# Kernel optimization log

Hardware: AMD Instinct MI355X
Metric: run time of the kernel (lower is better)

## Reference

```python
import jax, jax.numpy as jnp
import numpy as np

BNK, L, DIN, DOUT, NREL = 1280, 64, 512, 256, 40

def setup_inputs() -> dict:
    key = jax.random.key(0)
    ks = jax.random.split(key, 10)
    rep = jax.random.normal(ks[0], (BNK, L, DIN), dtype=jnp.float32)
    # adj_arc_in[..., 0] = flattened sentence index, adj_arc_in[..., 1] = head token position
    sent = jnp.broadcast_to(jnp.arange(BNK, dtype=jnp.int64)[:, None], (BNK, L))
    head = jax.random.randint(ks[1], (BNK, L), 0, L, dtype=jnp.int64)
    adj_arc_in = jnp.stack([sent, head], axis=-1)  # [BNK, L, 2]
    adj_lab_in = jax.random.randint(ks[2], (BNK, L), 0, NREL, dtype=jnp.int64)
    adj_mask_in = (jax.random.uniform(ks[3], (BNK, L)) < 0.9).astype(jnp.float32)
    adj_mask_loop = jnp.ones((BNK, L), dtype=jnp.float32)
    mask = jnp.ones((BNK, L), dtype=jnp.float32)
    # parameters (xavier-ish init)
    W_in = jax.random.normal(ks[4], (DIN, DOUT), dtype=jnp.float32) * (2.0 / (DIN + DOUT)) ** 0.5
    b_in = jnp.zeros((NREL, DOUT), dtype=jnp.float32)
    W_gate_in = jax.random.uniform(ks[5], (DIN, 1), dtype=jnp.float32)
    b_gate_in = jnp.ones((NREL, 1), dtype=jnp.float32)
    W_self = jax.random.normal(ks[6], (DIN, DOUT), dtype=jnp.float32) * (2.0 / (DIN + DOUT)) ** 0.5
    W_gate_self = jax.random.uniform(ks[7], (DIN, 1), dtype=jnp.float32)
    return {"rep": rep, "adj_mask_in": adj_mask_in, "adj_mask_loop": adj_mask_loop,
            "mask": mask, "W_in": W_in, "b_in": b_in, "W_gate_in": W_gate_in,
            "b_gate_in": b_gate_in, "W_self": W_self, "W_gate_self": W_gate_self,
            "adj_arc_in": adj_arc_in, "adj_lab_in": adj_lab_in}

def reference(rep, adj_mask_in, adj_mask_loop, mask, W_in, b_in, W_gate_in,
              b_gate_in, W_self, W_gate_self, adj_arc_in, adj_lab_in):
    bnk, l, din = rep.shape
    dout = W_in.shape[1]
    rep_ = rep.reshape(bnk * l, din)                    # [M, Din]
    idx = adj_arc_in[..., 0].reshape(-1) * l + adj_arc_in[..., 1].reshape(-1)  # [M]
    lab = adj_lab_in.reshape(-1)                        # [M]
    # in-arc potential: gather projected head token, add relation-typed bias
    in_pot = (rep_ @ W_in)[idx] + b_in[lab]             # [M, Dout]
    in_gate = (rep_ @ W_gate_in)[idx, 0] + b_gate_in[lab, 0]  # [M]
    # self-loop potential
    self_pot = rep_ @ W_self                            # [M, Dout]
    self_gate = (rep_ @ W_gate_self)[:, 0]              # [M]
    pots = jnp.stack([in_pot, self_pot], axis=1)        # [M, 2, Dout]
    gates = jnp.stack([in_gate, self_gate], axis=1)     # [M, 2]
    msoft = jnp.stack([adj_mask_in.reshape(-1), adj_mask_loop.reshape(-1)], axis=1)  # [M, 2]
    # original multiplies by mask_soft twice: potentials * mask_soft * (sigmoid(gate) * mask_soft)
    w = jax.nn.sigmoid(gates) * msoft * msoft           # [M, 2]
    res = jax.nn.relu(jnp.einsum('mdk,md->mk', pots, w))  # [M, Dout]
    res = res.reshape(bnk, l, dout) * mask.reshape(bnk, l)[..., None]
    return res
```

## Files before the change

kernel.cpp:

```cpp
#include <hip/hip_runtime.h>


#define BNK   1280
#define LTOK  64
#define DIN   512
#define DOUT  256
#define NCAT  512
#define TPB   512
#define BK    32
#define NCHUNK (DIN / BK)
#define A_STRIDE 56

typedef __attribute__((ext_vector_type(4))) float f32x4;
typedef __attribute__((ext_vector_type(8))) short s16x8;

__device__ __forceinline__ unsigned short f2bf(float f) {
  unsigned u = __float_as_uint(f);
  unsigned r = (u + 0x7FFFu + ((u >> 16) & 1u)) >> 16;
  return (unsigned short)r;
}
__device__ __forceinline__ float bf2f(unsigned short h) {
  return __uint_as_float(((unsigned)h) << 16);
}
__device__ __forceinline__ float sigmoidf_(float x) {
  return 1.0f / (1.0f + __expf(-x));
}

__global__ __launch_bounds__(256) void wprep_kernel(const float* __restrict__ W_in,
                                                    const float* __restrict__ W_self,
                                                    unsigned short* __restrict__ Wt) {
  __shared__ float tile[32][33];
  const int t  = threadIdx.x;
  const int c0 = (blockIdx.x & 15) * 32;
  const int k0 = (blockIdx.x >> 4) * 32;
  const float* src = (c0 < DOUT) ? W_in : W_self;
  const int cadj   = (c0 < DOUT) ? c0 : (c0 - DOUT);
  {
    const int kk = t >> 3;
    const int cc = (t & 7) * 4;
    const float4 v = *(const float4*)(src + (size_t)(k0 + kk) * DOUT + cadj + cc);
    tile[kk][cc + 0] = v.x; tile[kk][cc + 1] = v.y;
    tile[kk][cc + 2] = v.z; tile[kk][cc + 3] = v.w;
  }
  __syncthreads();
  {
    const int cc = t >> 3;
    const int kk = (t & 7) * 4;
    ushort4 o;
    o.x = f2bf(tile[kk + 0][cc]); o.y = f2bf(tile[kk + 1][cc]);
    o.z = f2bf(tile[kk + 2][cc]); o.w = f2bf(tile[kk + 3][cc]);
    *(ushort4*)(Wt + (size_t)(c0 + cc) * DIN + k0 + kk) = o;
  }
}

__global__ __launch_bounds__(TPB) void gcn_kernel(
    const float* __restrict__ rep,
    const float* __restrict__ adj_mask_in,
    const float* __restrict__ adj_mask_loop,
    const float* __restrict__ maskp,
    const float* __restrict__ b_in,
    const float* __restrict__ w_gate_in,
    const float* __restrict__ b_gate_in,
    const float* __restrict__ w_gate_self,
    const int* __restrict__ arc,
    const int* __restrict__ lab,
    const unsigned short* __restrict__ Wt,
    float* __restrict__ out)
{
  __shared__ __align__(16) char smem[41728];
  unsigned short* As  = (unsigned short*)(smem);
  unsigned short* Ws  = (unsigned short*)(smem + 7168);
  unsigned short* Pin = (unsigned short*)(smem);
  unsigned short* Psf = (unsigned short*)(smem + 16384);
  float* wgi  = (float*)(smem);
  float* wgs  = (float*)(smem + 2048);
  float* part = (float*)(smem + 4096);
  float* gld  = (float*)(smem + 39936);
  float* winl = (float*)(smem + 40448);
  float* wsfl = (float*)(smem + 40704);
  float* mskl = (float*)(smem + 40960);
  int*   hdl  = (int*)(smem + 41216);
  int*   lbl  = (int*)(smem + 41472);

  const int b    = blockIdx.x;
  const int t    = threadIdx.x;
  const int wave = t >> 6;
  const int lane = t & 63;
  const int nlo  = lane & 15;
  const int quad = lane >> 4;

  wgi[t] = w_gate_in[t];
  wgs[t] = w_gate_self[t];
  __syncthreads();
  {
    const int r = t >> 3, p = t & 7;
    const float* row = rep + (size_t)(b * LTOK + r) * DIN;
    float si = 0.f, ss = 0.f;
    #pragma unroll 8
    for (int j = 0; j < 64; ++j) {
      const int k = p + j * 8;
      const float a = row[k];
      si += a * wgi[k];
      ss += a * wgs[k];
    }
    part[t * 2 + 0] = si;
    part[t * 2 + 1] = ss;
  }
  __syncthreads();
  if (t < 128) {
    const int r = t >> 1, g = t & 1;
    float s = 0.f;
    #pragma unroll
    for (int p = 0; p < 8; ++p) s += part[(r * 8 + p) * 2 + g];
    gld[r * 2 + g] = s;
  }

  f32x4 acc[4][4];
  #pragma unroll
  for (int i = 0; i < 4; ++i)
    #pragma unroll
    for (int j = 0; j < 4; ++j) {
      f32x4 z = {0.f, 0.f, 0.f, 0.f};
      acc[i][j] = z;
    }

  for (int kc = 0; kc < NCHUNK; ++kc) {
    __syncthreads();
    const int k0 = kc * BK;

    #pragma unroll
    for (int i = 0; i < 4; ++i) {
      const int u = i * TPB + t;
      const int c = u >> 2;
      const int p = u & 3;
      const int q = p ^ ((c >> 1) & 3);
      const unsigned short* g = Wt + (size_t)c * DIN + k0 + q * 8;
      __builtin_amdgcn_global_load_lds(
          (const __attribute__((address_space(1))) void*)g,
          (__attribute__((address_space(3))) void*)(smem + 7168 + u * 16),
          16, 0, 0);
    }

    {
      const int r  = t >> 3;
      const int kk = (t & 7) * 4;
      const float4 v = *(const float4*)(rep + (size_t)(b * LTOK + r) * DIN + k0 + kk);
      ushort4 o;
      o.x = f2bf(v.x); o.y = f2bf(v.y); o.z = f2bf(v.z); o.w = f2bf(v.w);
      *(ushort4*)(As + r * A_STRIDE + kk) = o;
    }
    __syncthreads();

    s16x8 af[4];
    #pragma unroll
    for (int mt = 0; mt < 4; ++mt)
      af[mt] = *(const s16x8*)(As + (mt * 16 + nlo) * A_STRIDE + quad * 8);

    #pragma unroll
    for (int nt = 0; nt < 4; ++nt) {
      const int c = wave * 64 + nt * 16 + nlo;
      const int p = quad ^ ((c >> 1) & 3);
      const s16x8 bfr = *(const s16x8*)(Ws + c * BK + p * 8);
      #pragma unroll
      for (int mt = 0; mt < 4; ++mt)
        acc[mt][nt] = __builtin_amdgcn_mfma_f32_16x16x32_bf16(af[mt], bfr, acc[mt][nt], 0, 0, 0);
    }
  }

  __syncthreads();

  if (t < LTOK) {
    const int m  = b * LTOK + t;
    const int hd = arc[2 * m + 1];
    const int lb = lab[m];
    const float am = adj_mask_in[m];
    const float al = adj_mask_loop[m];
    winl[t] = sigmoidf_(gld[hd * 2 + 0] + b_gate_in[lb]) * am * am;
    wsfl[t] = sigmoidf_(gld[t * 2 + 1]) * al * al;
    mskl[t] = maskp[m];
    hdl[t]  = hd;
    lbl[t]  = lb;
  }

  for (int s = 0; s < 2; ++s) {
    if (s) __syncthreads();
    const int half = wave >> 2;
    const int wcol = wave & 3;
    if ((wcol >> 1) == s) {
      unsigned short* dst = half ? Psf : Pin;
      const int cb = (wcol & 1) * 64;
      #pragma unroll
      for (int mt = 0; mt < 4; ++mt)
        #pragma unroll
        for (int nt = 0; nt < 4; ++nt)
          #pragma unroll
          for (int r = 0; r < 4; ++r) {
            const int row = mt * 16 + quad * 4 + r;
            const int col = cb + nt * 16 + nlo;
            dst[row * 128 + col] = f2bf(acc[mt][nt][r]);
          }
    }
    __syncthreads();
    #pragma unroll
    for (int i = 0; i < 4; ++i) {
      const int q   = i * TPB + t;
      const int row = q >> 5;
      const int cl  = (q & 31) * 4;
      const int cg  = s * 128 + cl;
      const int hd  = hdl[row];
      const int lb  = lbl[row];
      const float wi = winl[row], ws = wsfl[row], mk = mskl[row];
      const float4 bi = *(const float4*)(b_in + lb * DOUT + cg);
      const ushort4 pi = *(const ushort4*)(Pin + hd * 128 + cl);
      const ushort4 ps = *(const ushort4*)(Psf + row * 128 + cl);
      float4 v;
      v.x = (bf2f(pi.x) + bi.x) * wi + bf2f(ps.x) * ws;
      v.y = (bf2f(pi.y) + bi.y) * wi + bf2f(ps.y) * ws;
      v.z = (bf2f(pi.z) + bi.z) * wi + bf2f(ps.z) * ws;
      v.w = (bf2f(pi.w) + bi.w) * wi + bf2f(ps.w) * ws;
      v.x = fmaxf(v.x, 0.f) * mk; v.y = fmaxf(v.y, 0.f) * mk;
      v.z = fmaxf(v.z, 0.f) * mk; v.w = fmaxf(v.w, 0.f) * mk;
      *(float4*)(out + (size_t)(b * LTOK + row) * DOUT + cg) = v;
    }
  }
}

extern "C" void kernel_launch(void* const* d_in, const int* in_sizes, int n_in,
                              void* d_out, int out_size, void* d_ws, size_t ws_size,
                              hipStream_t stream) {
  const float* rep           = (const float*)d_in[0];
  const float* adj_mask_in   = (const float*)d_in[1];
  const float* adj_mask_loop = (const float*)d_in[2];
  const float* mask          = (const float*)d_in[3];
  const float* W_in          = (const float*)d_in[4];
  const float* b_in          = (const float*)d_in[5];
  const float* W_gate_in     = (const float*)d_in[6];
  const float* b_gate_in     = (const float*)d_in[7];
  const float* W_self        = (const float*)d_in[8];
  const float* W_gate_self   = (const float*)d_in[9];
  const int*   arc           = (const int*)d_in[10];
  const int*   lab           = (const int*)d_in[11];
  float* out = (float*)d_out;
  unsigned short* Wt = (unsigned short*)d_ws;

  wprep_kernel<<<256, 256, 0, stream>>>(W_in, W_self, Wt);
  gcn_kernel<<<BNK, TPB, 0, stream>>>(rep, adj_mask_in, adj_mask_loop, mask, b_in,
                                      W_gate_in, b_gate_in, W_gate_self, arc, lab, Wt, out);
}
```

Measured before the change: 378.7 us.

## Stage full A tile once in LDS and stream W fragments directly from global

The gate-dot pass now also converts each rep row to bf16 and stores the whole 64x512 A tile in swizzled LDS in the same read, so the per-chunk rep reload and conversion inside the K loop go away. B fragments are read straight from global/L2 into registers instead of being staged through LDS with per-chunk barriers, so the K loop has no syncthreads and is fully unrolled. The epilogue writes both projections into LDS with a padded stride in a single pass rather than two halves. The kernel uses more shared memory (about 77KB) and relies on L2 bandwidth for the repeated W reads, with a launch-bounds occupancy hint added.

Result: faster. 357.6 us (-5.6%).

```diff
diff --git a/kernel.cpp b/kernel.cpp
--- a/kernel.cpp
+++ b/kernel.cpp
@@ -5,11 +5,10 @@
 #define LTOK  64
 #define DIN   512
 #define DOUT  256
-#define NCAT  512
 #define TPB   512
-#define BK    32
-#define NCHUNK (DIN / BK)
-#define A_STRIDE 56
+#define PSTR  264
+
+#define SMEM_BYTES 77568
 
 typedef __attribute__((ext_vector_type(4))) float f32x4;
 typedef __attribute__((ext_vector_type(8))) short s16x8;
@@ -53,7 +52,7 @@
   }
 }
 
-__global__ __launch_bounds__(TPB) void gcn_kernel(
+__global__ __launch_bounds__(TPB, 4) void gcn_kernel(
     const float* __restrict__ rep,
     const float* __restrict__ adj_mask_in,
     const float* __restrict__ adj_mask_loop,
@@ -67,20 +66,19 @@
     const unsigned short* __restrict__ Wt,
     float* __restrict__ out)
 {
-  __shared__ __align__(16) char smem[41728];
+  __shared__ __align__(16) char smem[SMEM_BYTES];
   unsigned short* As  = (unsigned short*)(smem);
-  unsigned short* Ws  = (unsigned short*)(smem + 7168);
   unsigned short* Pin = (unsigned short*)(smem);
-  unsigned short* Psf = (unsigned short*)(smem + 16384);
-  float* wgi  = (float*)(smem);
-  float* wgs  = (float*)(smem + 2048);
-  float* part = (float*)(smem + 4096);
-  float* gld  = (float*)(smem + 39936);
-  float* winl = (float*)(smem + 40448);
-  float* wsfl = (float*)(smem + 40704);
-  float* mskl = (float*)(smem + 40960);
-  int*   hdl  = (int*)(smem + 41216);
-  int*   lbl  = (int*)(smem + 41472);
+  unsigned short* Psf = (unsigned short*)(smem + 33792);
+  float* wgi  = (float*)(smem + 67584);
+  float* wgs  = (float*)(smem + 69632);
+  float* part = (float*)(smem + 71680);
+  float* gld  = (float*)(smem + 75776);
+  float* winl = (float*)(smem + 76288);
+  float* wsfl = (float*)(smem + 76544);
+  float* mskl = (float*)(smem + 76800);
+  int*   hdl  = (int*)(smem + 77056);
+  int*   lbl  = (int*)(smem + 77312);
 
   const int b    = blockIdx.x;
   const int t    = threadIdx.x;
@@ -92,21 +90,38 @@
   wgi[t] = w_gate_in[t];
   wgs[t] = w_gate_self[t];
   __syncthreads();
+
   {
     const int r = t >> 3, p = t & 7;
-    const float* row = rep + (size_t)(b * LTOK + r) * DIN;
+    const float* arow = rep + (size_t)(b * LTOK + r) * DIN;
     float si = 0.f, ss = 0.f;
-    #pragma unroll 8
-    for (int j = 0; j < 64; ++j) {
-      const int k = p + j * 8;
-      const float a = row[k];
-      si += a * wgi[k];
-      ss += a * wgs[k];
+    #pragma unroll 4
+    for (int i = 0; i < 8; ++i) {
+      const int kg = p + 8 * i;
+      const int kb = kg * 8;
+      const float4 v0 = *(const float4*)(arow + kb);
+      const float4 v1 = *(const float4*)(arow + kb + 4);
+      const float4 g0 = *(const float4*)(wgi + kb);
+      const float4 g1 = *(const float4*)(wgi + kb + 4);
+      const float4 h0 = *(const float4*)(wgs + kb);
+      const float4 h1 = *(const float4*)(wgs + kb + 4);
+      si += v0.x*g0.x + v0.y*g0.y + v0.z*g0.z + v0.w*g0.w
+          + v1.x*g1.x + v1.y*g1.y + v1.z*g1.z + v1.w*g1.w;
+      ss += v0.x*h0.x + v0.y*h0.y + v0.z*h0.z + v0.w*h0.w
+          + v1.x*h1.x + v1.y*h1.y + v1.z*h1.z + v1.w*h1.w;
+      s16x8 o;
+      o[0] = (short)f2bf(v0.x); o[1] = (short)f2bf(v0.y);
+      o[2] = (short)f2bf(v0.z); o[3] = (short)f2bf(v0.w);
+      o[4] = (short)f2bf(v1.x); o[5] = (short)f2bf(v1.y);
+      o[6] = (short)f2bf(v1.z); o[7] = (short)f2bf(v1.w);
+      const int u = (kg >> 2) * 256 + (kg & 3) * 64 + (r ^ p);
+      *(s16x8*)(As + u * 8) = o;
     }
     part[t * 2 + 0] = si;
     part[t * 2 + 1] = ss;
   }
   __syncthreads();
+
   if (t < 128) {
     const int r = t >> 1, g = t & 1;
     float s = 0.f;
@@ -124,47 +139,26 @@
       acc[i][j] = z;
     }
 
-  for (int kc = 0; kc < NCHUNK; ++kc) {
-    __syncthreads();
-    const int k0 = kc * BK;
-
-    #pragma unroll
-    for (int i = 0; i < 4; ++i) {
-      const int u = i * TPB + t;
-      const int c = u >> 2;
-      const int p = u & 3;
-      const int q = p ^ ((c >> 1) & 3);
-      const unsigned short* g = Wt + (size_t)c * DIN + k0 + q * 8;
-      __builtin_amdgcn_global_load_lds(
-          (const __attribute__((address_space(1))) void*)g,
-          (__attribute__((address_space(3))) void*)(smem + 7168 + u * 16),
-          16, 0, 0);
-    }
-
-    {
-      const int r  = t >> 3;
-      const int kk = (t & 7) * 4;
-      const float4 v = *(const float4*)(rep + (size_t)(b * LTOK + r) * DIN + k0 + kk);
-      ushort4 o;
-      o.x = f2bf(v.x); o.y = f2bf(v.y); o.z = f2bf(v.z); o.w = f2bf(v.w);
-      *(ushort4*)(As + r * A_STRIDE + kk) = o;
-    }
-    __syncthreads();
-
-    s16x8 af[4];
+  const unsigned short* aeven = As + (quad * 64 + (nlo ^ quad)) * 8;
+  const unsigned short* aodd  = As + (quad * 64 + (nlo ^ (quad + 4))) * 8;
+  const unsigned short* wb = Wt + (size_t)(wave * 64 + nlo) * DIN + quad * 8;
+
+  #pragma unroll
+  for (int kc = 0; kc < 16; ++kc) {
+    const unsigned short* ab = ((kc & 1) ? aodd : aeven) + kc * 2048;
+    const unsigned short* wk = wb + kc * 32;
+    s16x8 af[4], bf[4];
     #pragma unroll
     for (int mt = 0; mt < 4; ++mt)
-      af[mt] = *(const s16x8*)(As + (mt * 16 + nlo) * A_STRIDE + quad * 8);
-
-    #pragma unroll
-    for (int nt = 0; nt < 4; ++nt) {
-      const int c = wave * 64 + nt * 16 + nlo;
-      const int p = quad ^ ((c >> 1) & 3);
-      const s16x8 bfr = *(const s16x8*)(Ws + c * BK + p * 8);
+      af[mt] = *(const s16x8*)(ab + mt * 128);
+    #pragma unroll
+    for (int nt = 0; nt < 4; ++nt)
+      bf[nt] = *(const s16x8*)(wk + nt * 16 * DIN);
+    #pragma unroll
+    for (int nt = 0; nt < 4; ++nt)
       #pragma unroll
       for (int mt = 0; mt < 4; ++mt)
-        acc[mt][nt] = __builtin_amdgcn_mfma_f32_16x16x32_bf16(af[mt], bfr, acc[mt][nt], 0, 0, 0);
-    }
+        acc[mt][nt] = __builtin_amdgcn_mfma_f32_16x16x32_bf16(af[mt], bf[nt], acc[mt][nt], 0, 0, 0);
   }
 
   __syncthreads();
@@ -182,46 +176,40 @@
     lbl[t]  = lb;
   }
 
-  for (int s = 0; s < 2; ++s) {
-    if (s) __syncthreads();
-    const int half = wave >> 2;
-    const int wcol = wave & 3;
-    if ((wcol >> 1) == s) {
-      unsigned short* dst = half ? Psf : Pin;
-      const int cb = (wcol & 1) * 64;
+  {
+    unsigned short* dst = (wave < 4) ? Pin : Psf;
+    const int cb = (wave & 3) * 64;
+    #pragma unroll
+    for (int mt = 0; mt < 4; ++mt)
       #pragma unroll
-      for (int mt = 0; mt < 4; ++mt)
+      for (int nt = 0; nt < 4; ++nt)
         #pragma unroll
-        for (int nt = 0; nt < 4; ++nt)
-          #pragma unroll
-          for (int r = 0; r < 4; ++r) {
-            const int row = mt * 16 + quad * 4 + r;
-            const int col = cb + nt * 16 + nlo;
-            dst[row * 128 + col] = f2bf(acc[mt][nt][r]);
-          }
-    }
-    __syncthreads();
-    #pragma unroll
-    for (int i = 0; i < 4; ++i) {
-      const int q   = i * TPB + t;
-      const int row = q >> 5;
-      const int cl  = (q & 31) * 4;
-      const int cg  = s * 128 + cl;
-      const int hd  = hdl[row];
-      const int lb  = lbl[row];
-      const float wi = winl[row], ws = wsfl[row], mk = mskl[row];
-      const float4 bi = *(const float4*)(b_in + lb * DOUT + cg);
-      const ushort4 pi = *(const ushort4*)(Pin + hd * 128 + cl);
-      const ushort4 ps = *(const ushort4*)(Psf + row * 128 + cl);
-      float4 v;
-      v.x = (bf2f(pi.x) + bi.x) * wi + bf2f(ps.x) * ws;
-      v.y = (bf2f(pi.y) + bi.y) * wi + bf2f(ps.y) * ws;
-      v.z = (bf2f(pi.z) + bi.z) * wi + bf2f(ps.z) * ws;
-      v.w = (bf2f(pi.w) + bi.w) * wi + bf2f(ps.w) * ws;
-      v.x = fmaxf(v.x, 0.f) * mk; v.y = fmaxf(v.y, 0.f) * mk;
-      v.z = fmaxf(v.z, 0.f) * mk; v.w = fmaxf(v.w, 0.f) * mk;
-      *(float4*)(out + (size_t)(b * LTOK + row) * DOUT + cg) = v;
-    }
+        for (int rr = 0; rr < 4; ++rr) {
+          const int row = mt * 16 + quad * 4 + rr;
+          const int col = cb + nt * 16 + nlo;
+          dst[row * PSTR + col] = f2bf(acc[mt][nt][rr]);
+        }
+  }
+  __syncthreads();
+
+  #pragma unroll
+  for (int i = 0; i < 8; ++i) {
+    const int row = i * 8 + wave;
+    const int cl  = (t & 63) * 4;
+    const int hd  = hdl[row];
+    const int lb  = lbl[row];
+    const float wi = winl[row], ws = wsfl[row], mk = mskl[row];
+    const float4  bi = *(const float4*)(b_in + lb * DOUT + cl);
+    const ushort4 pi = *(const ushort4*)(Pin + hd * PSTR + cl);
+    const ushort4 ps = *(const ushort4*)(Psf + row * PSTR + cl);
+    float4 v;
+    v.x = (bf2f(pi.x) + bi.x) * wi + bf2f(ps.x) * ws;
+    v.y = (bf2f(pi.y) + bi.y) * wi + bf2f(ps.y) * ws;
+    v.z = (bf2f(pi.z) + bi.z) * wi + bf2f(ps.z) * ws;
+    v.w = (bf2f(pi.w) + bi.w) * wi + bf2f(ps.w) * ws;
+    v.x = fmaxf(v.x, 0.f) * mk; v.y = fmaxf(v.y, 0.f) * mk;
+    v.z = fmaxf(v.z, 0.f) * mk; v.w = fmaxf(v.w, 0.f) * mk;
+    *(float4*)(out + (size_t)(b * LTOK + row) * DOUT + cl) = v;
   }
 }
 
```
